# Performance work log

Measured on AMD Instinct MI355X. Metric: run time of the kernel, lower is better.

The kernel has to match this reference:

```python
import jax, jax.numpy as jnp
import numpy as np

M, N, F = 512, 128, 512  # molecules, atoms per molecule, feature dim
HID, OUT = F // 4, 1


def setup_inputs() -> dict:
    key = jax.random.key(0)
    k1, k2, k3 = jax.random.split(key, 3)
    h = jax.random.normal(k1, (M, N, F), dtype=jnp.float32)
    W1 = jax.random.normal(k2, (F, HID), dtype=jnp.float32) * (1.0 / np.sqrt(F))
    b1 = jnp.zeros((HID,), dtype=jnp.float32)
    W2 = jax.random.normal(k3, (HID, OUT), dtype=jnp.float32) * (1.0 / np.sqrt(HID))
    b2 = jnp.zeros((OUT,), dtype=jnp.float32)
    return {"h": h, "W1": W1, "b1": b1, "W2": W2, "b2": b2}


def reference(h, W1, b1, W2, b2):
    # method == 'weighted_summation'
    # gate MLP: Linear -> ReLU -> Linear -> Sigmoid, per atom
    w = jax.nn.sigmoid(jax.nn.relu(h @ W1 + b1) @ W2 + b2)  # [M, N, OUT]
    # per-molecule weighted sum over atoms: mm(w_h.T, h) for each molecule,
    # concatenated along dim 0 -> [M*OUT, F] (OUT=1 -> [M, F])
    out = jnp.einsum('mno,mnf->mof', w, h)  # [M, OUT, F]
    return out.reshape(M * OUT, F)
```

## Files before the change

### kernel.cpp

```cpp
#include <hip/hip_runtime.h>
#include <hip/hip_bf16.h>


typedef unsigned short u16;
typedef unsigned int u32;
typedef __bf16 bf16x8 __attribute__((ext_vector_type(8)));
typedef float f32x4 __attribute__((ext_vector_type(4)));
typedef u32 u32x4 __attribute__((ext_vector_type(4)));

#define M_MOL 512
#define N_ATOM 128
#define F_DIM 512
#define HID_DIM 128

static __device__ __forceinline__ u16 f2bf(float x) {
  u32 u = __float_as_uint(x);
  u32 r = (u + 0x7fffu + ((u >> 16) & 1u)) >> 16;
  return (u16)r;
}
static __device__ __forceinline__ bf16x8 pack8(u32x4 a, u32x4 b) {
  u32x4 r;
  r[0] = (a[0] >> 16) | (a[1] & 0xffff0000u);
  r[1] = (a[2] >> 16) | (a[3] & 0xffff0000u);
  r[2] = (b[0] >> 16) | (b[1] & 0xffff0000u);
  r[3] = (b[2] >> 16) | (b[3] & 0xffff0000u);
  return __builtin_bit_cast(bf16x8, r);
}

__global__ __launch_bounds__(256) void transpose_w1(const float* __restrict__ W1,
                                                    u16* __restrict__ W1Tt) {
  __shared__ float tile[64][65];
  const int k0 = blockIdx.x * 64;
  const int n0 = blockIdx.y * 64;
  const int t = threadIdx.x;
  #pragma unroll
  for (int i = 0; i < 16; ++i) {
    const int lin = i * 256 + t;
    const int lr = lin >> 6, lc = lin & 63;
    tile[lc][lr] = W1[(size_t)(k0 + lr) * HID_DIM + (n0 + lc)];
  }
  __syncthreads();
  #pragma unroll
  for (int i = 0; i < 16; ++i) {
    const int lin = i * 256 + t;
    const int wr = lin >> 6, wc = lin & 63;
    const int k = k0 + wc;
    W1Tt[(size_t)(k >> 5) * (HID_DIM * 32) + (size_t)(n0 + wr) * 32 + (k & 31)] =
        f2bf(tile[wr][wc]);
  }
}

__global__ __launch_bounds__(512, 2) void pool_mol(
    const float* __restrict__ h, const u16* __restrict__ W1Tt,
    const float* __restrict__ b1, const float* __restrict__ W2,
    const float* __restrict__ b2, float* __restrict__ out) {
  __shared__ u16 Bs[16 * HID_DIM * 32];
  __shared__ float red[8][F_DIM];
  __shared__ float w_s[N_ATOM];

  const int m = blockIdx.x;
  const int tid = threadIdx.x;
  const int wv = tid >> 6;
  const int lane = tid & 63;
  const int quad = lane >> 4;
  const int cl = lane & 15;

  {
    const u32x4* src = (const u32x4*)W1Tt;
    u32x4* dst = (u32x4*)Bs;
    #pragma unroll
    for (int i = 0; i < 16; ++i)
      dst[i * 512 + tid] = src[i * 512 + tid];
  }

  const int row = wv * 16 + cl;
  const float* hr = h + ((size_t)m * N_ATOM + row) * F_DIM;
  const u32x4* ap = (const u32x4*)hr + quad * 2;
  bf16x8 ah[16];
  {
    u32x4 a32[32];
    #pragma unroll
    for (int ks = 0; ks < 16; ++ks) {
      a32[2 * ks]     = ap[ks * 8];
      a32[2 * ks + 1] = ap[ks * 8 + 1];
    }
    #pragma unroll
    for (int ks = 0; ks < 16; ++ks)
      ah[ks] = pack8(a32[2 * ks], a32[2 * ks + 1]);
  }
  __syncthreads();

  f32x4 acc[8];
  #pragma unroll
  for (int t = 0; t < 8; ++t) acc[t] = (f32x4){0.f, 0.f, 0.f, 0.f};

  #pragma unroll
  for (int ks = 0; ks < 16; ++ks) {
    const u16* bt = Bs + ks * (HID_DIM * 32) + cl * 32 + quad * 8;
    #pragma unroll
    for (int t = 0; t < 8; ++t) {
      bf16x8 bfr = *(const bf16x8*)(bt + t * 512);
      acc[t] = __builtin_amdgcn_mfma_f32_16x16x32_bf16(ah[ks], bfr, acc[t], 0, 0, 0);
    }
  }

  float psum[4] = {0.f, 0.f, 0.f, 0.f};
  #pragma unroll
  for (int t = 0; t < 8; ++t) {
    const int hid = t * 16 + cl;
    const float b1v = b1[hid];
    const float w2v = W2[hid];
    #pragma unroll
    for (int r = 0; r < 4; ++r) {
      float tv = fmaxf(acc[t][r] + b1v, 0.f);
      psum[r] = fmaf(tv, w2v, psum[r]);
    }
  }
  #pragma unroll
  for (int off = 1; off < 16; off <<= 1)
    #pragma unroll
    for (int r = 0; r < 4; ++r)
      psum[r] += __shfl_xor(psum[r], off, 64);
  if (cl == 0) {
    const float b2v = b2[0];
    #pragma unroll
    for (int r = 0; r < 4; ++r)
      w_s[wv * 16 + quad * 4 + r] = 1.f / (1.f + __expf(-(psum[r] + b2v)));
  }
  asm volatile("s_waitcnt lgkmcnt(0)" ::: "memory");
  __builtin_amdgcn_sched_barrier(0);

  const float wn = w_s[wv * 16 + cl];
  float fout[8];
  #pragma unroll
  for (int ks = 0; ks < 16; ++ks) {
    u32x4 uv = __builtin_bit_cast(u32x4, ah[ks]);
    float p[8];
    #pragma unroll
    for (int j = 0; j < 4; ++j) {
      p[2 * j]     = wn * __uint_as_float(uv[j] << 16);
      p[2 * j + 1] = wn * __uint_as_float(uv[j] & 0xffff0000u);
    }
    #pragma unroll
    for (int off = 1; off < 16; off <<= 1)
      #pragma unroll
      for (int j = 0; j < 8; ++j)
        p[j] += __shfl_xor(p[j], off, 64);
    if (cl == ks) {
      #pragma unroll
      for (int j = 0; j < 8; ++j) fout[j] = p[j];
    }
  }

  #pragma unroll
  for (int j = 0; j < 8; ++j) red[wv][cl * 32 + quad * 8 + j] = fout[j];
  __syncthreads();

  {
    const int f = tid;
    float o = 0.f;
    #pragma unroll
    for (int w = 0; w < 8; ++w) o += red[w][f];
    out[(size_t)m * F_DIM + f] = o;
  }
}

extern "C" void kernel_launch(void* const* d_in, const int* in_sizes, int n_in,
                              void* d_out, int out_size, void* d_ws, size_t ws_size,
                              hipStream_t stream) {
  const float* h  = (const float*)d_in[0];
  const float* W1 = (const float*)d_in[1];
  const float* b1 = (const float*)d_in[2];
  const float* W2 = (const float*)d_in[3];
  const float* b2 = (const float*)d_in[4];
  float* out = (float*)d_out;

  u16* W1Tt = (u16*)d_ws;

  transpose_w1<<<dim3(8, 2), 256, 0, stream>>>(W1, W1Tt);
  pool_mol<<<M_MOL, 512, 0, stream>>>(h, W1Tt, b1, W2, b2, out);
}
```

Measured before the change: 226.0 us.

## Stream W1 fragments from global with triple-buffered registers and stage h in LDS

Drops the LDS staging of the whole transposed W1 and instead prefetches W1 B-fragments straight from global memory into a three-slot register ring two k-steps ahead of the MFMAs. The LDS freed by this holds the bf16-packed h tile with an XOR swizzle. The weighted sum over atoms then becomes per-lane FMAs over rows read from LDS, replacing the 16-round shuffle-reduction butterfly. The cost is heavier register use and repeated global/L2 reads of W1 per block, and the 128 KB As buffer likely lowers occupancy. There is also no barrier between the As writes and the cross-lane reads, though each wave reads only its own rows.

```diff
diff --git a/kernel.cpp b/kernel.cpp
--- a/kernel.cpp
+++ b/kernel.cpp
@@ -54,7 +54,7 @@
     const float* __restrict__ h, const u16* __restrict__ W1Tt,
     const float* __restrict__ b1, const float* __restrict__ W2,
     const float* __restrict__ b2, float* __restrict__ out) {
-  __shared__ u16 Bs[16 * HID_DIM * 32];
+  __shared__ u16 As[N_ATOM * F_DIM];
   __shared__ float red[8][F_DIM];
   __shared__ float w_s[N_ATOM];
 
@@ -65,30 +65,32 @@
   const int quad = lane >> 4;
   const int cl = lane & 15;
 
-  {
-    const u32x4* src = (const u32x4*)W1Tt;
-    u32x4* dst = (u32x4*)Bs;
-    #pragma unroll
-    for (int i = 0; i < 16; ++i)
-      dst[i * 512 + tid] = src[i * 512 + tid];
-  }
-
   const int row = wv * 16 + cl;
   const float* hr = h + ((size_t)m * N_ATOM + row) * F_DIM;
   const u32x4* ap = (const u32x4*)hr + quad * 2;
+  u32x4 a32[16][2];
+  #pragma unroll
+  for (int ks = 0; ks < 16; ++ks) {
+    a32[ks][0] = ap[ks * 8];
+    a32[ks][1] = ap[ks * 8 + 1];
+  }
+
+  const u16* bg = W1Tt + cl * 32 + quad * 8;
+  u32x4 bf[3][8];
+  #pragma unroll
+  for (int p = 0; p < 2; ++p)
+    #pragma unroll
+    for (int t = 0; t < 8; ++t)
+      bf[p][t] = *(const u32x4*)(bg + (size_t)p * (HID_DIM * 32) + t * 512);
+
   bf16x8 ah[16];
-  {
-    u32x4 a32[32];
-    #pragma unroll
-    for (int ks = 0; ks < 16; ++ks) {
-      a32[2 * ks]     = ap[ks * 8];
-      a32[2 * ks + 1] = ap[ks * 8 + 1];
-    }
-    #pragma unroll
-    for (int ks = 0; ks < 16; ++ks)
-      ah[ks] = pack8(a32[2 * ks], a32[2 * ks + 1]);
+  #pragma unroll
+  for (int ks = 0; ks < 16; ++ks) {
+    ah[ks] = pack8(a32[ks][0], a32[ks][1]);
+    const int c = ks * 4 + quad;
+    const int phys = (c & ~7) | ((c ^ cl) & 7);
+    *(bf16x8*)(As + row * F_DIM + phys * 8) = ah[ks];
   }
-  __syncthreads();
 
   f32x4 acc[8];
   #pragma unroll
@@ -96,12 +98,16 @@
 
   #pragma unroll
   for (int ks = 0; ks < 16; ++ks) {
-    const u16* bt = Bs + ks * (HID_DIM * 32) + cl * 32 + quad * 8;
+    if (ks < 14) {
+      #pragma unroll
+      for (int t = 0; t < 8; ++t)
+        bf[(ks + 2) % 3][t] =
+            *(const u32x4*)(bg + (size_t)(ks + 2) * (HID_DIM * 32) + t * 512);
+    }
     #pragma unroll
-    for (int t = 0; t < 8; ++t) {
-      bf16x8 bfr = *(const bf16x8*)(bt + t * 512);
-      acc[t] = __builtin_amdgcn_mfma_f32_16x16x32_bf16(ah[ks], bfr, acc[t], 0, 0, 0);
-    }
+    for (int t = 0; t < 8; ++t)
+      acc[t] = __builtin_amdgcn_mfma_f32_16x16x32_bf16(
+          ah[ks], __builtin_bit_cast(bf16x8, bf[ks % 3][t]), acc[t], 0, 0, 0);
   }
 
   float psum[4] = {0.f, 0.f, 0.f, 0.f};
@@ -130,30 +136,23 @@
   asm volatile("s_waitcnt lgkmcnt(0)" ::: "memory");
   __builtin_amdgcn_sched_barrier(0);
 
-  const float wn = w_s[wv * 16 + cl];
-  float fout[8];
-  #pragma unroll
-  for (int ks = 0; ks < 16; ++ks) {
-    u32x4 uv = __builtin_bit_cast(u32x4, ah[ks]);
-    float p[8];
+  float facc[8] = {0.f, 0.f, 0.f, 0.f, 0.f, 0.f, 0.f, 0.f};
+  #pragma unroll 4
+  for (int i = 0; i < 16; ++i) {
+    const int r = wv * 16 + i;
+    const float wn = w_s[r];
+    const int phys = (lane & ~7) | ((lane ^ i) & 7);
+    bf16x8 hv = *(const bf16x8*)(As + r * F_DIM + phys * 8);
+    u32x4 uv = __builtin_bit_cast(u32x4, hv);
     #pragma unroll
     for (int j = 0; j < 4; ++j) {
-      p[2 * j]     = wn * __uint_as_float(uv[j] << 16);
-      p[2 * j + 1] = wn * __uint_as_float(uv[j] & 0xffff0000u);
-    }
-    #pragma unroll
-    for (int off = 1; off < 16; off <<= 1)
-      #pragma unroll
-      for (int j = 0; j < 8; ++j)
-        p[j] += __shfl_xor(p[j], off, 64);
-    if (cl == ks) {
-      #pragma unroll
-      for (int j = 0; j < 8; ++j) fout[j] = p[j];
+      facc[2 * j]     = fmaf(wn, __uint_as_float(uv[j] << 16), facc[2 * j]);
+      facc[2 * j + 1] = fmaf(wn, __uint_as_float(uv[j] & 0xffff0000u), facc[2 * j + 1]);
     }
   }
 
   #pragma unroll
-  for (int j = 0; j < 8; ++j) red[wv][cl * 32 + quad * 8 + j] = fout[j];
+  for (int j = 0; j < 8; ++j) red[wv][lane * 8 + j] = facc[j];
   __syncthreads();
 
   {
```

Result: faster. 207.1 us (median of 2 runs) (-8.4%).
